# Performance work log

Hardware: AMD Instinct MI355X
Metric: run time of the kernel (lower is better)

Reference implementation:

```python
import jax, jax.numpy as jnp
import numpy as np

N_SEGMENT = 8
NUM_HEADS = 4
KERNEL = 5
PAD_L = 4  # causal left padding (kernel_size - 1)


def setup_inputs() -> dict:
    key = jax.random.key(0)
    k1, k2 = jax.random.split(key)
    x = jax.random.normal(k1, (128, 512, 14, 14), dtype=jnp.float32)
    W_weight = jax.random.normal(k2, (NUM_HEADS * KERNEL, 512), dtype=jnp.float32) * 0.02
    return {"x": x, "W_weight": W_weight}


def reference(x, W_weight):
    nt, c, h, w = x.shape
    T = N_SEGMENT
    n = nt // T
    B = n * h * w
    H, K, R = NUM_HEADS, KERNEL, c // NUM_HEADS

    # (nt, c, h, w) -> (n, T, c, h, w) -> permute(1,0,3,4,2) -> (T, B, c)
    xt = x.reshape(n, T, c, h, w).transpose(1, 0, 3, 4, 2).reshape(T, B, c)

    # per-position dynamic kernels: Linear(c -> H*K), softmax over kernel taps
    w_logits = jnp.einsum('tbc,oc->tbo', xt, W_weight).reshape(T, B, H, K)
    weights = jax.nn.softmax(w_logits, axis=-1)  # (T, B, H, K)

    # causal banded unfold: window[t, ..., k] = x[t + k - PAD_L], zeros outside
    xpad = jnp.pad(xt, ((PAD_L, 0), (0, 0), (0, 0)))  # (T+4, B, c)
    windows = jnp.stack([xpad[k:k + T] for k in range(K)], axis=-1)  # (T, B, c, K)
    win = windows.reshape(T, B, H, R, K)

    out = jnp.einsum('tbhrk,tbhk->tbhr', win, weights).reshape(T, B, c)

    # (T, n, h, w, c) -> permute(1,0,4,2,3) -> (nt, c, h, w)
    out = out.reshape(T, n, h, w, c).transpose(1, 0, 4, 2, 3).reshape(nt, c, h, w)
    return out
```

## Files before the change

kernel.cpp:

```cpp
#include <hip/hip_runtime.h>

#define T 8
#define C 512
#define HW 196
#define NSEG 16
#define NT (NSEG * T)
#define B_TOT (NSEG * HW)
#define NH 4
#define KK 5
#define NO 20
#define S_SPLIT 8
#define CCH (C / S_SPLIT)

__global__ __launch_bounds__(256) void k_logits(const float* __restrict__ x,
                                                const float* __restrict__ W,
                                                float* __restrict__ pl) {
    const int idx = blockIdx.x * 256 + threadIdx.x;
    const int nt  = idx / HW;
    const int hw  = idx - nt * HW;
    const int s   = blockIdx.y;
    const int cbase = s * CCH;

    const float* xp = x + ((size_t)nt * C + cbase) * HW + hw;

    float acc[NO];
#pragma unroll
    for (int o = 0; o < NO; ++o) acc[o] = 0.f;

    float xv[8], xn[8];
#pragma unroll
    for (int u = 0; u < 8; ++u) xv[u] = xp[u * HW];

#pragma unroll
    for (int c0 = 0; c0 < CCH; c0 += 8) {
        if (c0 + 8 < CCH) {
#pragma unroll
            for (int u = 0; u < 8; ++u) xn[u] = xp[(c0 + 8 + u) * HW];
        }
        const float* wr = W + cbase + c0;
#pragma unroll
        for (int o = 0; o < NO; ++o) {
#pragma unroll
            for (int u = 0; u < 8; ++u)
                acc[o] = fmaf(xv[u], wr[o * C + u], acc[o]);
        }
#pragma unroll
        for (int u = 0; u < 8; ++u) xv[u] = xn[u];
    }

    float* pp = pl + ((size_t)(s * NT + nt) * NO) * HW + hw;
#pragma unroll
    for (int o = 0; o < NO; ++o) pp[o * HW] = acc[o];
}

__global__ __launch_bounds__(256) void k_softmax(const float* __restrict__ pl,
                                                 float* __restrict__ wgt) {
    const int b = blockIdx.x * 256 + threadIdx.x;
    const int t = blockIdx.y;
    const int h = blockIdx.z;
    if (b >= B_TOT) return;
    const int n  = b / HW;
    const int hw = b - n * HW;
    const int nt = n * T + t;

    float lg[KK];
#pragma unroll
    for (int k = 0; k < KK; ++k) {
        float sm = 0.f;
#pragma unroll
        for (int s = 0; s < S_SPLIT; ++s)
            sm += pl[((size_t)(s * NT + nt) * NO + h * KK + k) * HW + hw];
        lg[k] = sm;
    }

    float m = lg[0];
#pragma unroll
    for (int k = 1; k < KK; ++k) m = fmaxf(m, lg[k]);
    float e[KK];
    float sum = 0.f;
#pragma unroll
    for (int k = 0; k < KK; ++k) {
        e[k] = __expf(lg[k] - m);
        sum += e[k];
    }
    const float r = 1.f / sum;
#pragma unroll
    for (int k = 0; k < KK; ++k)
        wgt[((size_t)((t * NH + h) * KK + k)) * B_TOT + b] = e[k] * r;
}

__global__ __launch_bounds__(256) void k_conv(const float* __restrict__ x,
                                              const float* __restrict__ wgt,
                                              float* __restrict__ out) {
    const int idx = blockIdx.x * 256 + threadIdx.x;
    const int hw  = idx % HW;
    const int t1  = idx / HW;
    const int c   = t1 % C;
    const int n   = t1 / C;
    const int h   = c >> 7;
    const int b   = n * HW + hw;

    float w[T][KK];
#pragma unroll
    for (int t = 0; t < T; ++t)
#pragma unroll
        for (int k = 0; k < KK; ++k)
            w[t][k] = wgt[((size_t)((t * NH + h) * KK + k)) * B_TOT + b];

    const size_t base = ((size_t)(n * T) * C + c) * HW + hw;
    float xv[T];
#pragma unroll
    for (int t = 0; t < T; ++t) xv[t] = x[base + (size_t)t * C * HW];

#pragma unroll
    for (int t = 0; t < T; ++t) {
        float acc = 0.f;
#pragma unroll
        for (int k = 0; k < KK; ++k) {
            const int j = t + k - 4;
            if (j >= 0) acc = fmaf(w[t][k], xv[j], acc);
        }
        out[base + (size_t)t * C * HW] = acc;
    }
}

extern "C" void kernel_launch(void* const* d_in, const int* in_sizes, int n_in,
                              void* d_out, int out_size, void* d_ws, size_t ws_size,
                              hipStream_t stream) {
    const float* x = (const float*)d_in[0];
    const float* W = (const float*)d_in[1];
    float* out = (float*)d_out;

    float* pl  = (float*)d_ws;
    float* wgt = pl + (size_t)S_SPLIT * NT * NO * HW;

    k_logits<<<dim3(25088 / 256, S_SPLIT), 256, 0, stream>>>(x, W, pl);
    k_softmax<<<dim3((B_TOT + 255) / 256, T, NH), 256, 0, stream>>>(pl, wgt);
    k_conv<<<dim3((NSEG * C * HW) / 256), 256, 0, stream>>>(x, wgt, out);
}
```

Measured before the change: 125.8 us.

## Stage logits input via LDS async loads and vectorize softmax and conv with float4

The logits kernel now streams x into double-buffered shared memory using global_load_lds async copies, with a barrier per chunk. The softmax and conv kernels are rewritten so each thread handles four consecutive spatial positions using float4 loads and stores. The conv kernel also processes two channels per thread, so each softmax weight load serves two channels. This targets instruction count and memory transaction overhead, at the cost of per-chunk barriers, higher register use and fewer threads.

```diff
diff --git a/kernel.cpp b/kernel.cpp
--- a/kernel.cpp
+++ b/kernel.cpp
@@ -12,40 +12,55 @@
 #define S_SPLIT 8
 #define CCH (C / S_SPLIT)
 
+typedef const __attribute__((address_space(1))) unsigned int g_u32;
+typedef __attribute__((address_space(3))) unsigned int l_u32;
+
 __global__ __launch_bounds__(256) void k_logits(const float* __restrict__ x,
                                                 const float* __restrict__ W,
                                                 float* __restrict__ pl) {
-    const int idx = blockIdx.x * 256 + threadIdx.x;
+    const int tid = threadIdx.x;
+    const int idx = blockIdx.x * 256 + tid;
     const int nt  = idx / HW;
     const int hw  = idx - nt * HW;
     const int s   = blockIdx.y;
     const int cbase = s * CCH;
+    const int wave  = tid >> 6;
+
+    __shared__ float lds[2][8][256];
 
     const float* xp = x + ((size_t)nt * C + cbase) * HW + hw;
+
+#pragma unroll
+    for (int u = 0; u < 8; ++u)
+        __builtin_amdgcn_global_load_lds((g_u32*)(xp + u * HW),
+                                         (l_u32*)&lds[0][u][wave * 64], 4, 0, 0);
 
     float acc[NO];
 #pragma unroll
     for (int o = 0; o < NO; ++o) acc[o] = 0.f;
 
-    float xv[8], xn[8];
-#pragma unroll
-    for (int u = 0; u < 8; ++u) xv[u] = xp[u * HW];
+    __syncthreads();
 
 #pragma unroll
-    for (int c0 = 0; c0 < CCH; c0 += 8) {
-        if (c0 + 8 < CCH) {
+    for (int ch = 0; ch < 8; ++ch) {
+        const int buf = ch & 1;
+        if (ch + 1 < 8) {
 #pragma unroll
-            for (int u = 0; u < 8; ++u) xn[u] = xp[(c0 + 8 + u) * HW];
+            for (int u = 0; u < 8; ++u)
+                __builtin_amdgcn_global_load_lds(
+                    (g_u32*)(xp + ((ch + 1) * 8 + u) * HW),
+                    (l_u32*)&lds[buf ^ 1][u][wave * 64], 4, 0, 0);
         }
-        const float* wr = W + cbase + c0;
+        float xv[8];
 #pragma unroll
-        for (int o = 0; o < NO; ++o) {
+        for (int u = 0; u < 8; ++u) xv[u] = lds[buf][u][tid];
+        const float* wr = W + cbase + ch * 8;
+#pragma unroll
+        for (int o = 0; o < NO; ++o)
 #pragma unroll
             for (int u = 0; u < 8; ++u)
                 acc[o] = fmaf(xv[u], wr[o * C + u], acc[o]);
-        }
-#pragma unroll
-        for (int u = 0; u < 8; ++u) xv[u] = xn[u];
+        __syncthreads();
     }
 
     float* pp = pl + ((size_t)(s * NT + nt) * NO) * HW + hw;
@@ -55,72 +70,93 @@
 
 __global__ __launch_bounds__(256) void k_softmax(const float* __restrict__ pl,
                                                  float* __restrict__ wgt) {
-    const int b = blockIdx.x * 256 + threadIdx.x;
-    const int t = blockIdx.y;
-    const int h = blockIdx.z;
-    if (b >= B_TOT) return;
-    const int n  = b / HW;
-    const int hw = b - n * HW;
-    const int nt = n * T + t;
+    const int flat = blockIdx.x * 256 + threadIdx.x;
+    const int b4   = flat % (B_TOT / 4);
+    const int th   = flat / (B_TOT / 4);
+    const int h    = th & 3;
+    const int t    = th >> 2;
+    const int b    = b4 * 4;
+    const int n    = b / HW;
+    const int hw   = b - n * HW;
+    const int nt   = n * T + t;
 
-    float lg[KK];
+    float lg[KK][4];
 #pragma unroll
     for (int k = 0; k < KK; ++k) {
-        float sm = 0.f;
+        float s0 = 0.f, s1 = 0.f, s2 = 0.f, s3 = 0.f;
 #pragma unroll
-        for (int s = 0; s < S_SPLIT; ++s)
-            sm += pl[((size_t)(s * NT + nt) * NO + h * KK + k) * HW + hw];
-        lg[k] = sm;
+        for (int s = 0; s < S_SPLIT; ++s) {
+            const float4 v = *(const float4*)&pl[((size_t)(s * NT + nt) * NO + h * KK + k) * HW + hw];
+            s0 += v.x; s1 += v.y; s2 += v.z; s3 += v.w;
+        }
+        lg[k][0] = s0; lg[k][1] = s1; lg[k][2] = s2; lg[k][3] = s3;
     }
 
-    float m = lg[0];
+    float wv[KK][4];
 #pragma unroll
-    for (int k = 1; k < KK; ++k) m = fmaxf(m, lg[k]);
-    float e[KK];
-    float sum = 0.f;
+    for (int j = 0; j < 4; ++j) {
+        float m = lg[0][j];
+#pragma unroll
+        for (int k = 1; k < KK; ++k) m = fmaxf(m, lg[k][j]);
+        float e[KK];
+        float sum = 0.f;
+#pragma unroll
+        for (int k = 0; k < KK; ++k) { e[k] = __expf(lg[k][j] - m); sum += e[k]; }
+        const float r = 1.f / sum;
+#pragma unroll
+        for (int k = 0; k < KK; ++k) wv[k][j] = e[k] * r;
+    }
+
 #pragma unroll
     for (int k = 0; k < KK; ++k) {
-        e[k] = __expf(lg[k] - m);
-        sum += e[k];
+        const float4 o4 = make_float4(wv[k][0], wv[k][1], wv[k][2], wv[k][3]);
+        *(float4*)&wgt[((size_t)((t * NH + h) * KK + k)) * B_TOT + b] = o4;
     }
-    const float r = 1.f / sum;
-#pragma unroll
-    for (int k = 0; k < KK; ++k)
-        wgt[((size_t)((t * NH + h) * KK + k)) * B_TOT + b] = e[k] * r;
 }
 
 __global__ __launch_bounds__(256) void k_conv(const float* __restrict__ x,
                                               const float* __restrict__ wgt,
                                               float* __restrict__ out) {
-    const int idx = blockIdx.x * 256 + threadIdx.x;
-    const int hw  = idx % HW;
-    const int t1  = idx / HW;
-    const int c   = t1 % C;
-    const int n   = t1 / C;
-    const int h   = c >> 7;
-    const int b   = n * HW + hw;
+    const int flat = blockIdx.x * 256 + threadIdx.x;
+    const int q    = flat % 49;
+    const int rest = flat / 49;
+    const int cp   = rest & 255;
+    const int n    = rest >> 8;
+    const int c    = cp * 2;
+    const int h    = c >> 7;
+    const int hw   = q * 4;
+    const int b    = n * HW + hw;
 
-    float w[T][KK];
+    const size_t xbase = ((size_t)(n * T) * C + c) * HW + hw;
+
+    float4 xv[2][T];
 #pragma unroll
-    for (int t = 0; t < T; ++t)
-#pragma unroll
-        for (int k = 0; k < KK; ++k)
-            w[t][k] = wgt[((size_t)((t * NH + h) * KK + k)) * B_TOT + b];
-
-    const size_t base = ((size_t)(n * T) * C + c) * HW + hw;
-    float xv[T];
-#pragma unroll
-    for (int t = 0; t < T; ++t) xv[t] = x[base + (size_t)t * C * HW];
+    for (int t = 0; t < T; ++t) {
+        xv[0][t] = *(const float4*)&x[xbase + (size_t)t * C * HW];
+        xv[1][t] = *(const float4*)&x[xbase + (size_t)t * C * HW + HW];
+    }
 
 #pragma unroll
     for (int t = 0; t < T; ++t) {
-        float acc = 0.f;
+        float4 w4[KK];
 #pragma unroll
-        for (int k = 0; k < KK; ++k) {
-            const int j = t + k - 4;
-            if (j >= 0) acc = fmaf(w[t][k], xv[j], acc);
+        for (int k = 0; k < KK; ++k)
+            w4[k] = *(const float4*)&wgt[((size_t)((t * NH + h) * KK + k)) * B_TOT + b];
+#pragma unroll
+        for (int ci = 0; ci < 2; ++ci) {
+            float4 a = make_float4(0.f, 0.f, 0.f, 0.f);
+#pragma unroll
+            for (int k = 0; k < KK; ++k) {
+                const int j = t + k - 4;
+                if (j >= 0) {
+                    a.x = fmaf(w4[k].x, xv[ci][j].x, a.x);
+                    a.y = fmaf(w4[k].y, xv[ci][j].y, a.y);
+                    a.z = fmaf(w4[k].z, xv[ci][j].z, a.z);
+                    a.w = fmaf(w4[k].w, xv[ci][j].w, a.w);
+                }
+            }
+            *(float4*)&out[xbase + (size_t)t * C * HW + ci * HW] = a;
         }
-        out[base + (size_t)t * C * HW] = acc;
     }
 }
 
@@ -135,6 +171,6 @@
     float* wgt = pl + (size_t)S_SPLIT * NT * NO * HW;
 
     k_logits<<<dim3(25088 / 256, S_SPLIT), 256, 0, stream>>>(x, W, pl);
-    k_softmax<<<dim3((B_TOT + 255) / 256, T, NH), 256, 0, stream>>>(pl, wgt);
-    k_conv<<<dim3((NSEG * C * HW) / 256), 256, 0, stream>>>(x, wgt, out);
+    k_softmax<<<dim3(25088 / 256), 256, 0, stream>>>(pl, wgt);
+    k_conv<<<dim3((NSEG * 256 * 49) / 256), 256, 0, stream>>>(x, wgt, out);
 }
```

After: 145.7 us. 1.16x slower.
